# Kernel optimization log

Hardware: AMD Instinct MI355X
Metric: run time of the kernel (lower is better)

The kernel has to match this reference:

```python
import jax, jax.numpy as jnp
import numpy as np

N = 10000      # nodes
E = 160000     # edges (before self-loops)
H = 2          # ATTN_HEADS
D_IN = 256
C1 = 256       # hidden_channels per head in conv1
C2 = 512       # per-head channels in conv2 (hardcoded 512 in module)
OUT = 3


def setup_inputs():
    key = jax.random.key(0)
    ks = jax.random.split(key, 20)
    rn = lambda k, s, sc=0.05: jax.random.normal(k, s, jnp.float32) * sc
    return {
        "x": jax.random.normal(ks[0], (N, D_IN), jnp.float32),
        "edge_index": jax.random.randint(ks[1], (2, E), 0, N),
        # conv1: lin_src/lin_dst [D_IN, H*C1], attention vecs [H, C1], bias [H*C1]
        "w1s": rn(ks[2], (D_IN, H * C1)), "w1d": rn(ks[3], (D_IN, H * C1)),
        "a1s": rn(ks[4], (H, C1)), "a1d": rn(ks[5], (H, C1)), "b1": rn(ks[6], (H * C1,)),
        # conv2: input dim H*C1 -> [H*C1, H*C2]
        "w2s": rn(ks[7], (H * C1, H * C2)), "w2d": rn(ks[8], (H * C1, H * C2)),
        "a2s": rn(ks[9], (H, C2)), "a2d": rn(ks[10], (H, C2)), "b2": rn(ks[11], (H * C2,)),
        # MLP head
        "wf1": rn(ks[12], (H * C2, 128)), "bf1": rn(ks[13], (128,)),
        "gamma": jnp.ones((128,), jnp.float32), "beta": jnp.zeros((128,), jnp.float32),
        "wf2": rn(ks[14], (128, OUT)), "bf2": rn(ks[15], (OUT,)),
    }


def gat_layer(x, src, dst, Ws, Wd, att_s, att_d, b, n):
    h, c = att_s.shape
    xs = (x @ Ws).reshape(n, h, c)                      # [N,H,C] source messages
    xd = (x @ Wd).reshape(n, h, c)
    a_s = (xs * att_s).sum(-1)                          # [N,H]
    a_d = (xd * att_d).sum(-1)
    e = a_s[src] + a_d[dst]                             # [E,H]
    e = jnp.where(e > 0, e, 0.2 * e)                    # leaky_relu(0.2)
    m = jax.lax.stop_gradient(jax.ops.segment_max(e, dst, num_segments=n))
    alpha = jnp.exp(e - m[dst])
    denom = jax.ops.segment_sum(alpha, dst, num_segments=n)
    alpha = alpha / denom[dst]                          # segment softmax over dst
    out = jax.ops.segment_sum(xs[src] * alpha[..., None], dst, num_segments=n)
    return out.reshape(n, h * c) + b                    # concat heads + bias


def reference(x, edge_index, w1s, w1d, a1s, a1d, b1, w2s, w2d, a2s, a2d, b2,
              wf1, bf1, gamma, beta, wf2, bf2):
    loops = jnp.arange(N, dtype=edge_index.dtype)
    src = jnp.concatenate([edge_index[0], loops])       # add self-loops (PyG default)
    dst = jnp.concatenate([edge_index[1], loops])
    h = jax.nn.relu(gat_layer(x, src, dst, w1s, w1d, a1s, a1d, b1, N))
    h = jax.nn.relu(gat_layer(h, src, dst, w2s, w2d, a2s, a2d, b2, N))
    h = h @ wf1 + bf1
    mean = h.mean(0)
    var = ((h - mean) ** 2).mean(0)
    h = gamma * (h - mean) * jax.lax.rsqrt(var + 1e-5) + beta
    h = jax.nn.relu(h)
    h = h @ wf2 + bf2
    return jax.nn.log_softmax(h, axis=-1)
```

## Files before the change

kernel.cpp:

```cpp
#include <hip/hip_runtime.h>
#include <cstdint>
#include <cstddef>


typedef unsigned short u16;
typedef __bf16 bf16x8 __attribute__((ext_vector_type(8)));
typedef float f32x4 __attribute__((ext_vector_type(4)));
typedef unsigned short u16x8 __attribute__((ext_vector_type(8)));

__device__ __forceinline__ u16 f2b(float f) {
  union { float f; uint32_t u; } c; c.f = f;
  uint32_t u = c.u;
  return (u16)((u + 0x7FFFu + ((u >> 16) & 1u)) >> 16);
}
__device__ __forceinline__ float b2f(u16 h) {
  union { uint32_t u; float f; } c; c.u = ((uint32_t)h) << 16;
  return c.f;
}

__device__ __forceinline__ void async16(const void* g, void* l) {
  __builtin_amdgcn_global_load_lds((const __attribute__((address_space(1))) void*)g,
                                   (__attribute__((address_space(3))) void*)l, 16, 0, 0);
}

__device__ __forceinline__ float2 edge_w(const float4& as, const float4& ad) {
  float e0 = as.x + ad.z; e0 = e0 > 0.f ? e0 : 0.2f * e0;
  float e1 = as.y + ad.w; e1 = e1 > 0.f ? e1 : 0.2f * e1;
  return make_float2(__expf(e0), __expf(e1));
}

__device__ __forceinline__ void transpose_tile(const float* __restrict__ W, u16* __restrict__ WT,
                                               int K, int NC, int b, int t,
                                               u16 (*tile)[66]) {
  int tn = NC >> 6;
  int ti = b / tn, tj = b - ti * tn;
  int col = t & 63, r0 = t >> 6;
  const float* src = W + (size_t)(ti * 64) * NC + tj * 64;
#pragma unroll
  for (int i = 0; i < 16; i++) {
    int r = r0 + i * 4;
    tile[r][col] = f2b(src[(size_t)r * NC + col]);
  }
  __syncthreads();
  u16* dst = WT + (size_t)(tj * 64) * K + ti * 64;
#pragma unroll
  for (int i = 0; i < 16; i++) {
    int r = r0 + i * 4;
    dst[(size_t)r * K + col] = tile[col][r];
  }
}

__global__ __launch_bounds__(256) void prep(
    const float* __restrict__ x,
    const float* __restrict__ w1s, const float* __restrict__ w1d,
    const float* __restrict__ w2s, const float* __restrict__ w2d,
    const float* __restrict__ wf1,
    const float* __restrict__ a1s, const float* __restrict__ a1d,
    const float* __restrict__ a2s, const float* __restrict__ a2d,
    u16* __restrict__ xb, u16* __restrict__ w1T, u16* __restrict__ w2T,
    u16* __restrict__ wf1T, float* __restrict__ V1, float* __restrict__ V2,
    uint32_t* __restrict__ arena, int arena_nwords, int za,
    uint32_t* __restrict__ g1pad, int g1w, int zg1,
    uint32_t* __restrict__ g2pad, int g2w,
    int N) {
  __shared__ u16 tile[64][66];
  int b = blockIdx.x, t = threadIdx.x;
  const int R0 = 32;
  const int R1 = R0 + 128;
  const int R2 = R1 + 32;
  const int R3 = R2 + 256;
  const int R4 = R3 + 512;
  const int R5 = R4 + N / 4;
  const int R6 = R5 + za;
  const int R7 = R6 + zg1;

  if (b < R0) {
    transpose_tile(w1s, w1T, 256, 512, b, t, tile);
  } else if (b < R1) {
    transpose_tile(w2s, w2T, 512, 1024, b - R0, t, tile);
  } else if (b < R2) {
    transpose_tile(wf1, wf1T, 1024, 128, b - R1, t, tile);
  } else if (b < R3) {
    int wv = t >> 6, lane = t & 63;
    int u = (b - R2) * 4 + wv;
    int k = u >> 2, which = (u >> 1) & 1, h = u & 1;
    const float* W = which ? w1d : w1s;
    const float* att = which ? a1d : a1s;
    float s = 0.f;
#pragma unroll
    for (int c = lane; c < 256; c += 64) s += W[k * 512 + h * 256 + c] * att[h * 256 + c];
#pragma unroll
    for (int o = 32; o > 0; o >>= 1) s += __shfl_down(s, o);
    if (lane == 0) V1[k * 4 + which * 2 + h] = s;
  } else if (b < R4) {
    int wv = t >> 6, lane = t & 63;
    int u = (b - R3) * 4 + wv;
    int k = u >> 2, which = (u >> 1) & 1, h = u & 1;
    const float* W = which ? w2d : w2s;
    const float* att = which ? a2d : a2s;
    float s = 0.f;
#pragma unroll
    for (int c = lane; c < 512; c += 64) s += W[k * 1024 + h * 512 + c] * att[h * 512 + c];
#pragma unroll
    for (int o = 32; o > 0; o >>= 1) s += __shfl_down(s, o);
    if (lane == 0) V2[k * 4 + which * 2 + h] = s;
  } else if (b < R5) {
    int r = (b - R4) * 4 + (t >> 6);
    int c = (t & 63) * 4;
    float4 xv = *(const float4*)(x + (size_t)r * 256 + c);
    ushort4 st;
    st.x = f2b(xv.x); st.y = f2b(xv.y); st.z = f2b(xv.z); st.w = f2b(xv.w);
    *(ushort4*)(xb + (size_t)r * 256 + c) = st;
  } else if (b < R6) {
    int idx = (b - R5) * 256 + t;
    if (idx < arena_nwords) arena[idx] = 0u;
  } else if (b < R7) {
    int idx = (b - R6) * 256 + t;
    if (idx < g1w) g1pad[idx] = 0u;
  } else {
    int idx = (b - R7) * 256 + t;
    if (idx < g2w) g2pad[idx] = 0u;
  }
}

__global__ __launch_bounds__(256) void fill_a(const int* __restrict__ srcs,
                                              const int* __restrict__ dsts,
                                              int* __restrict__ cursor, int* __restrict__ csr,
                                              const float* __restrict__ X,
                                              const float* __restrict__ V,
                                              float* __restrict__ A, int N, int E, int FB) {
  int b = blockIdx.x, t = threadIdx.x;
  if (b < FB) {
    int i = b * 256 + t;
    if (i < N) {
      csr[(size_t)i * 64] = i;
    } else if (i < N + E) {
      int e = i - N;
      int d = dsts[e];
      int slot = atomicAdd(&cursor[d], 1) + 1;
      if (slot < 64) csr[(size_t)d * 64 + slot] = srcs[e];
    }
    return;
  }
  int node = (b - FB) * 4 + (t >> 6);
  int lane = t & 63;
  if (node >= N) return;
  const float* xr = X + (size_t)node * 256;
  float s0 = 0, s1 = 0, s2 = 0, s3 = 0;
  {
    int k = lane * 4;
    float4 xv = *(const float4*)(xr + k);
    float xe[4] = {xv.x, xv.y, xv.z, xv.w};
#pragma unroll
    for (int j = 0; j < 4; j++) {
      float4 v = ((const float4*)V)[k + j];
      s0 += xe[j] * v.x; s1 += xe[j] * v.y; s2 += xe[j] * v.z; s3 += xe[j] * v.w;
    }
  }
#pragma unroll
  for (int o = 32; o > 0; o >>= 1) {
    s0 += __shfl_down(s0, o); s1 += __shfl_down(s1, o);
    s2 += __shfl_down(s2, o); s3 += __shfl_down(s3, o);
  }
  if (lane == 0) ((float4*)A)[node] = make_float4(s0, s1, s2, s3);
}

__global__ __launch_bounds__(256) void agg1(const u16* __restrict__ xs,
                                            const float* __restrict__ a,
                                            const int* __restrict__ cursor,
                                            const int* __restrict__ csr,
                                            u16* __restrict__ g, int N) {
  int v = blockIdx.x * 8 + (threadIdx.x >> 5);
  if (v >= N) return;
  int c0 = (threadIdx.x & 31) * 8;
  const int* seg = csr + (size_t)v * 64;
  int cnt = min(cursor[v], 63) + 1;
  const float4* a4 = (const float4*)a;
  float4 adv = a4[v];
  float h0[8], h1[8];
#pragma unroll
  for (int j = 0; j < 8; j++) { h0[j] = 0.f; h1[j] = 0.f; }
  float den0 = 0.f, den1 = 0.f;

  auto body = [&](int4 s4) {
    float4 aa0 = a4[s4.x], aa1 = a4[s4.y], aa2 = a4[s4.z], aa3 = a4[s4.w];
    u16x8 x0 = *(const u16x8*)(xs + (size_t)s4.x * 256 + c0);
    u16x8 x1 = *(const u16x8*)(xs + (size_t)s4.y * 256 + c0);
    u16x8 x2 = *(const u16x8*)(xs + (size_t)s4.z * 256 + c0);
    u16x8 x3 = *(const u16x8*)(xs + (size_t)s4.w * 256 + c0);
    float2 w0 = edge_w(aa0, adv), w1 = edge_w(aa1, adv);
    float2 w2 = edge_w(aa2, adv), w3 = edge_w(aa3, adv);
    den0 += w0.x + w1.x + w2.x + w3.x;
    den1 += w0.y + w1.y + w2.y + w3.y;
#pragma unroll
    for (int j = 0; j < 8; j++) {
      float f0 = b2f(x0[j]), f1 = b2f(x1[j]), f2 = b2f(x2[j]), f3 = b2f(x3[j]);
      h0[j] += w0.x * f0 + w1.x * f1 + w2.x * f2 + w3.x * f3;
      h1[j] += w0.y * f0 + w1.y * f1 + w2.y * f2 + w3.y * f3;
    }
  };

  int nb4 = cnt & ~3;
  int i = 0;
  if (nb4 > 0) {
    int4 s4 = *(const int4*)(seg);
    for (i = 4; i < nb4; i += 4) {
      int4 nxt = *(const int4*)(seg + i);
      body(s4);
      s4 = nxt;
    }
    body(s4);
    i = nb4;
  }
  for (; i < cnt; i++) {
    int s = seg[i];
    float2 w = edge_w(a4[s], adv);
    den0 += w.x; den1 += w.y;
    u16x8 xv = *(const u16x8*)(xs + (size_t)s * 256 + c0);
#pragma unroll
    for (int j = 0; j < 8; j++) {
      float f = b2f(xv[j]);
      h0[j] += w.x * f;
      h1[j] += w.y * f;
    }
  }
  float r0 = 1.f / den0, r1 = 1.f / den1;
  u16x8 o0v, o1v;
#pragma unroll
  for (int j = 0; j < 8; j++) {
    o0v[j] = f2b(h0[j] * r0);
    o1v[j] = f2b(h1[j] * r1);
  }
  u16* grow = g + (size_t)v * 512;
  *(u16x8*)(grow + c0) = o0v;
  *(u16x8*)(grow + 256 + c0) = o1v;
}

__global__ __launch_bounds__(256) void agg2(const u16* __restrict__ xs,
                                            const float* __restrict__ a,
                                            const int* __restrict__ cursor,
                                            const int* __restrict__ csr,
                                            u16* __restrict__ g, int N) {
  int v = blockIdx.x * 4 + (threadIdx.x >> 6);
  if (v >= N) return;
  int c0 = (threadIdx.x & 63) * 8;
  const int* seg = csr + (size_t)v * 64;
  int cnt = min(cursor[v], 63) + 1;
  const float4* a4 = (const float4*)a;
  float4 adv = a4[v];
  float h0[8], h1[8];
#pragma unroll
  for (int j = 0; j < 8; j++) { h0[j] = 0.f; h1[j] = 0.f; }
  float den0 = 0.f, den1 = 0.f;

  auto body = [&](int4 s4) {
    float4 aa0 = a4[s4.x], aa1 = a4[s4.y], aa2 = a4[s4.z], aa3 = a4[s4.w];
    u16x8 x0 = *(const u16x8*)(xs + (size_t)s4.x * 512 + c0);
    u16x8 x1 = *(const u16x8*)(xs + (size_t)s4.y * 512 + c0);
    u16x8 x2 = *(const u16x8*)(xs + (size_t)s4.z * 512 + c0);
    u16x8 x3 = *(const u16x8*)(xs + (size_t)s4.w * 512 + c0);
    float2 w0 = edge_w(aa0, adv), w1 = edge_w(aa1, adv);
    float2 w2 = edge_w(aa2, adv), w3 = edge_w(aa3, adv);
    den0 += w0.x + w1.x + w2.x + w3.x;
    den1 += w0.y + w1.y + w2.y + w3.y;
#pragma unroll
    for (int j = 0; j < 8; j++) {
      float f0 = b2f(x0[j]), f1 = b2f(x1[j]), f2 = b2f(x2[j]), f3 = b2f(x3[j]);
      h0[j] += w0.x * f0 + w1.x * f1 + w2.x * f2 + w3.x * f3;
      h1[j] += w0.y * f0 + w1.y * f1 + w2.y * f2 + w3.y * f3;
    }
  };

  int nb4 = cnt & ~3;
  int i = 0;
  if (nb4 > 0) {
    int4 s4 = *(const int4*)(seg);
    for (i = 4; i < nb4; i += 4) {
      int4 nxt = *(const int4*)(seg + i);
      body(s4);
      s4 = nxt;
    }
    body(s4);
    i = nb4;
  }
  for (; i < cnt; i++) {
    int s = seg[i];
    float2 w = edge_w(a4[s], adv);
    den0 += w.x; den1 += w.y;
    u16x8 xv = *(const u16x8*)(xs + (size_t)s * 512 + c0);
#pragma unroll
    for (int j = 0; j < 8; j++) {
      float f = b2f(xv[j]);
      h0[j] += w.x * f;
      h1[j] += w.y * f;
    }
  }
  float r0 = 1.f / den0, r1 = 1.f / den1;
  u16x8 o0v, o1v;
#pragma unroll
  for (int j = 0; j < 8; j++) {
    o0v[j] = f2b(h0[j] * r0);
    o1v[j] = f2b(h1[j] * r1);
  }
  u16* grow = g + (size_t)v * 1024;
  *(u16x8*)(grow + c0) = o0v;
  *(u16x8*)(grow + 512 + c0) = o1v;
}

template <bool A2OUT>
__global__ __launch_bounds__(256) void gemm_bf16(const u16* __restrict__ A, int lda, int aZ,
                                                 const u16* __restrict__ BT, int ldb, int bZ,
                                                 const float* __restrict__ bias, int biasZ,
                                                 void* __restrict__ Cv, int ldc,
                                                 size_t cZ, int K, float* __restrict__ a2out,
                                                 const float* __restrict__ Vfold) {
  __shared__ u16 Asl[2][128 * 32];
  __shared__ u16 Bsl[2][128 * 32];
  int tid = threadIdx.x;
  int wave = tid >> 6, lane = tid & 63;
  int wr = wave >> 1, wc = wave & 1;
  int lr = lane & 15, quad = lane >> 4;
  size_t row0 = (size_t)blockIdx.y * 128;
  size_t n0 = (size_t)blockIdx.x * 128;
  int zq = blockIdx.z;
  A += (size_t)zq * aZ;
  BT += (size_t)zq * bZ;
  bias += (size_t)zq * biasZ;

  f32x4 acc[4][4];
#pragma unroll
  for (int i = 0; i < 4; i++)
#pragma unroll
    for (int j = 0; j < 4; j++) acc[i][j] = (f32x4){0.f, 0.f, 0.f, 0.f};

  int ra = tid >> 2;
  int ca = (tid & 3) * 8;
  const u16* gA = A + (row0 + ra) * lda + ca;
  const u16* gB = BT + (n0 + ra) * ldb + ca;
  int lbase = (tid & 192) * 8;

  async16(gA, &Asl[0][lbase]);
  async16(gA + (size_t)64 * lda, &Asl[0][lbase + 2048]);
  async16(gB, &Bsl[0][lbase]);
  async16(gB + (size_t)64 * ldb, &Bsl[0][lbase + 2048]);
  __syncthreads();

  int nIter = K >> 5;
  for (int it = 0; it < nIter; it++) {
    int cur = it & 1;
    if (it + 1 < nIter) {
      int kn = (it + 1) * 32;
      async16(gA + kn, &Asl[1 - cur][lbase]);
      async16(gA + (size_t)64 * lda + kn, &Asl[1 - cur][lbase + 2048]);
      async16(gB + kn, &Bsl[1 - cur][lbase]);
      async16(gB + (size_t)64 * ldb + kn, &Bsl[1 - cur][lbase + 2048]);
    }
    bf16x8 av[4], bv[4];
#pragma unroll
    for (int i = 0; i < 4; i++)
      av[i] = *(const bf16x8*)&Asl[cur][(wr * 64 + i * 16 + lr) * 32 + quad * 8];
#pragma unroll
    for (int j = 0; j < 4; j++)
      bv[j] = *(const bf16x8*)&Bsl[cur][(wc * 64 + j * 16 + lr) * 32 + quad * 8];
#pragma unroll
    for (int i = 0; i < 4; i++)
#pragma unroll
      for (int j = 0; j < 4; j++)
        acc[i][j] = __builtin_amdgcn_mfma_f32_16x16x32_bf16(av[i], bv[j], acc[i][j], 0, 0, 0);
    __syncthreads();
  }

  size_t crow = row0 + wr * 64 + quad * 4;
  size_t ccol = n0 + wc * 64 + lr;
  float bj[4];
#pragma unroll
  for (int j = 0; j < 4; j++) bj[j] = bias[ccol + j * 16];
  float4 vr[4];
  if (A2OUT) {
#pragma unroll
    for (int j = 0; j < 4; j++)
      vr[j] = ((const float4*)Vfold)[(size_t)zq * cZ + ccol + j * 16];
  }
  u16* C = (u16*)Cv + (size_t)zq * cZ;
#pragma unroll
  for (int i = 0; i < 4; i++) {
#pragma unroll
    for (int r = 0; r < 4; r++) {
      float pa0 = 0.f, pa1 = 0.f, pa2 = 0.f, pa3 = 0.f;
#pragma unroll
      for (int j = 0; j < 4; j++) {
        float val = fmaxf(acc[i][j][r] + bj[j], 0.f);
        C[(crow + i * 16 + r) * ldc + ccol + j * 16] = f2b(val);
        if (A2OUT) {
          pa0 += val * vr[j].x; pa1 += val * vr[j].y;
          pa2 += val * vr[j].z; pa3 += val * vr[j].w;
        }
      }
      if (A2OUT) {
#pragma unroll
        for (int o = 8; o > 0; o >>= 1) {
          pa0 += __shfl_down(pa0, o); pa1 += __shfl_down(pa1, o);
          pa2 += __shfl_down(pa2, o); pa3 += __shfl_down(pa3, o);
        }
        if (lr == 0) {
          float* ap = a2out + (crow + i * 16 + r) * 4;
          atomicAdd(ap + 0, pa0); atomicAdd(ap + 1, pa1);
          atomicAdd(ap + 2, pa2); atomicAdd(ap + 3, pa3);
        }
      }
    }
  }
}

__global__ __launch_bounds__(256) void gemm3_head(
    const u16* __restrict__ A, const u16* __restrict__ BT,
    float* __restrict__ sums, unsigned int* __restrict__ ctr,
    const float* __restrict__ gamma, const float* __restrict__ beta,
    const float* __restrict__ wf2, const float* __restrict__ bf2,
    float* __restrict__ out, int N, int nBlocks) {
  __shared__ u16 Asl[2][64 * 32];
  __shared__ u16 Bsl[2][128 * 32];
  __shared__ float part[2][64][3];
  int tid = threadIdx.x;
  int wave = tid >> 6, lane = tid & 63;
  int wr = wave >> 1, wc = wave & 1;
  int lr = lane & 15, quad = lane >> 4;
  size_t row0 = (size_t)blockIdx.x * 64;

  f32x4 acc[2][4];
#pragma unroll
  for (int i = 0; i < 2; i++)
#pragma unroll
    for (int j = 0; j < 4; j++) acc[i][j] = (f32x4){0.f, 0.f, 0.f, 0.f};

  const u16* gA = A + (row0 + (tid >> 2)) * 1024 + (tid & 3) * 8;
  const u16* gB = BT + (size_t)(tid >> 2) * 1024 + (tid & 3) * 8;
  int lb = (tid & 192) * 8;

  async16(gA, &Asl[0][lb]);
  async16(gB, &Bsl[0][lb]);
  async16(gB + 64 * 1024, &Bsl[0][2048 + lb]);
  __syncthreads();

  for (int it = 0; it < 32; it++) {
    int cur = it & 1;
    if (it + 1 < 32) {
      int kn = (it + 1) * 32;
      async16(gA + kn, &Asl[1 - cur][lb]);
      async16(gB + kn, &Bsl[1 - cur][lb]);
      async16(gB + 64 * 1024 + kn, &Bsl[1 - cur][2048 + lb]);
    }
    bf16x8 av[2], bv[4];
#pragma unroll
    for (int i = 0; i < 2; i++)
      av[i] = *(const bf16x8*)&Asl[cur][(wr * 32 + i * 16 + lr) * 32 + quad * 8];
#pragma unroll
    for (int j = 0; j < 4; j++)
      bv[j] = *(const bf16x8*)&Bsl[cur][(wc * 64 + j * 16 + lr) * 32 + quad * 8];
#pragma unroll
    for (int i = 0; i < 2; i++)
#pragma unroll
      for (int j = 0; j < 4; j++)
        acc[i][j] = __builtin_amdgcn_mfma_f32_16x16x32_bf16(av[i], bv[j], acc[i][j], 0, 0, 0);
    __syncthreads();
  }

  int ccol = wc * 64 + lr;
  float s1[4] = {0.f, 0.f, 0.f, 0.f}, s2[4] = {0.f, 0.f, 0.f, 0.f};
#pragma unroll
  for (int i = 0; i < 2; i++)
#pragma unroll
    for (int r = 0; r < 4; r++) {
      int row = (int)row0 + wr * 32 + i * 16 + quad * 4 + r;
      if (row < N) {
#pragma unroll
        for (int j = 0; j < 4; j++) {
          float v = acc[i][j][r];
          s1[j] += v; s2[j] += v * v;
        }
      }
    }
#pragma unroll
  for (int j = 0; j < 4; j++) {
#pragma unroll
    for (int o = 16; o < 64; o <<= 1) {
      s1[j] += __shfl_down(s1[j], o);
      s2[j] += __shfl_down(s2[j], o);
    }
  }
  if (quad == 0) {
#pragma unroll
    for (int j = 0; j < 4; j++) {
      atomicAdd(&sums[ccol + j * 16], s1[j]);
      atomicAdd(&sums[128 + ccol + j * 16], s2[j]);
    }
  }

  __syncthreads();
  if (tid == 0) {
    __threadfence();
    atomicAdd(ctr, 1u);
    while (__hip_atomic_load(ctr, __ATOMIC_ACQUIRE, __HIP_MEMORY_SCOPE_AGENT) <
           (unsigned)nBlocks) {
    }
  }
  __syncthreads();

  float inv = 1.f / (float)N;
  float mean[4], rstd[4], gm[4], bt[4], w3[4][3];
#pragma unroll
  for (int j = 0; j < 4; j++) {
    int col = ccol + j * 16;
    float sv = __hip_atomic_load(&sums[col], __ATOMIC_RELAXED, __HIP_MEMORY_SCOPE_AGENT);
    float qv = __hip_atomic_load(&sums[128 + col], __ATOMIC_RELAXED, __HIP_MEMORY_SCOPE_AGENT);
    mean[j] = sv * inv;
    float var = qv * inv - mean[j] * mean[j];
    rstd[j] = rsqrtf(var + 1e-5f);
    gm[j] = gamma[col]; bt[j] = beta[col];
    w3[j][0] = wf2[col * 3 + 0]; w3[j][1] = wf2[col * 3 + 1]; w3[j][2] = wf2[col * 3 + 2];
  }
#pragma unroll
  for (int i = 0; i < 2; i++)
#pragma unroll
    for (int r = 0; r < 4; r++) {
      float p0 = 0.f, p1 = 0.f, p2 = 0.f;
#pragma unroll
      for (int j = 0; j < 4; j++) {
        float h = gm[j] * (acc[i][j][r] - mean[j]) * rstd[j] + bt[j];
        h = fmaxf(h, 0.f);
        p0 += h * w3[j][0]; p1 += h * w3[j][1]; p2 += h * w3[j][2];
      }
#pragma unroll
      for (int o = 8; o > 0; o >>= 1) {
        p0 += __shfl_down(p0, o); p1 += __shfl_down(p1, o); p2 += __shfl_down(p2, o);
      }
      if (lr == 0) {
        int lrow = wr * 32 + i * 16 + quad * 4 + r;
        part[wc][lrow][0] = p0; part[wc][lrow][1] = p1; part[wc][lrow][2] = p2;
      }
    }
  __syncthreads();
  if (tid < 64) {
    int row = tid;
    if ((int)row0 + row < N) {
      float l0 = part[0][row][0] + part[1][row][0] + bf2[0];
      float l1 = part[0][row][1] + part[1][row][1] + bf2[1];
      float l2 = part[0][row][2] + part[1][row][2] + bf2[2];
      float mx = fmaxf(l0, fmaxf(l1, l2));
      float lse = mx + logf(__expf(l0 - mx) + __expf(l1 - mx) + __expf(l2 - mx));
      float* orow = out + ((size_t)row0 + row) * 3;
      orow[0] = l0 - lse; orow[1] = l1 - lse; orow[2] = l2 - lse;
    }
  }
}

extern "C" void kernel_launch(void* const* d_in, const int* in_sizes, int n_in,
                              void* d_out, int out_size, void* d_ws, size_t ws_size,
                              hipStream_t stream) {
  const float* x     = (const float*)d_in[0];
  const int*   ei    = (const int*)d_in[1];
  const float* w1s   = (const float*)d_in[2];
  const float* w1d   = (const float*)d_in[3];
  const float* a1s   = (const float*)d_in[4];
  const float* a1d   = (const float*)d_in[5];
  const float* b1    = (const float*)d_in[6];
  const float* w2s   = (const float*)d_in[7];
  const float* w2d   = (const float*)d_in[8];
  const float* a2s   = (const float*)d_in[9];
  const float* a2d   = (const float*)d_in[10];
  const float* b2    = (const float*)d_in[11];
  const float* wf1   = (const float*)d_in[12];
  const float* gamma = (const float*)d_in[14];
  const float* beta  = (const float*)d_in[15];
  const float* wf2   = (const float*)d_in[16];
  const float* bf2   = (const float*)d_in[17];
  float* out = (float*)d_out;

  const int N = in_sizes[0] / 256;
  const int E = in_sizes[1] / 2;
  const int Mpad = ((N + 127) / 128) * 128;
  (void)n_in; (void)out_size; (void)ws_size;

  char* ws = (char*)d_ws;
  size_t off = 0;
  auto alloc = [&](size_t bytes) -> char* {
    off = (off + 255) & ~(size_t)255;
    char* p = ws + off;
    off += bytes;
    return p;
  };
  u16* xb    = (u16*)alloc((size_t)N * 256 * 2);
  u16* w1T   = (u16*)alloc((size_t)512 * 256 * 2);
  u16* w2T   = (u16*)alloc((size_t)1024 * 512 * 2);
  u16* wf1T  = (u16*)alloc((size_t)128 * 1024 * 2);
  u16* g1    = (u16*)alloc((size_t)Mpad * 512 * 2);
  u16* h1    = (u16*)alloc((size_t)Mpad * 512 * 2);
  u16* g2    = (u16*)alloc((size_t)Mpad * 1024 * 2);
  u16* h2    = (u16*)alloc((size_t)Mpad * 1024 * 2);
  float* a1  = (float*)alloc((size_t)N * 16);
  float* V1  = (float*)alloc(256 * 16);
  float* V2  = (float*)alloc(512 * 16);
  int* csr   = (int*)alloc((size_t)N * 64 * 4);
  size_t curB = (size_t)N * 4;
  size_t a2B = (size_t)Mpad * 16;
  size_t arenaB = curB + a2B + 1024 + 256;
  char* arena = alloc(arenaB);
  int* cursor = (int*)arena;
  float* a2   = (float*)(arena + curB);
  float* sums = (float*)(arena + curB + a2B);
  unsigned int* ctr = (unsigned int*)(sums + 256);

  int arena_nwords = (int)(arenaB / 4);
  int za  = (arena_nwords + 255) / 256;
  int g1w = (Mpad - N) * 512 * 2 / 4;
  int zg1 = (g1w + 255) / 256;
  int g2w = (Mpad - N) * 1024 * 2 / 4;
  int zg2 = (g2w + 255) / 256;
  int prep_blocks = 32 + 128 + 32 + 256 + 512 + N / 4 + za + zg1 + zg2;

  prep<<<prep_blocks, 256, 0, stream>>>(
      x, w1s, w1d, w2s, w2d, wf1, a1s, a1d, a2s, a2d,
      xb, w1T, w2T, wf1T, V1, V2,
      (uint32_t*)arena, arena_nwords, za,
      (uint32_t*)(g1 + (size_t)N * 512), g1w, zg1,
      (uint32_t*)(g2 + (size_t)N * 1024), g2w, N);

  const int* srcs = ei;
  const int* dsts = ei + E;

  int FB = (N + E + 255) / 256;
  fill_a<<<FB + (N + 3) / 4, 256, 0, stream>>>(srcs, dsts, cursor, csr, x, V1, a1, N, E, FB);

  int mt = Mpad / 128;

  agg1<<<(N + 7) / 8, 256, 0, stream>>>(xb, a1, cursor, csr, g1, N);
  gemm_bf16<true><<<dim3(2, mt, 2), 256, 0, stream>>>(
      g1, 512, 256, w1T, 256, 256 * 256, b1, 256, h1, 512, 256, 256, a2, V2);
  agg2<<<(N + 3) / 4, 256, 0, stream>>>(h1, a2, cursor, csr, g2, N);
  gemm_bf16<false><<<dim3(4, mt, 2), 256, 0, stream>>>(
      g2, 1024, 512, w2T, 512, 512 * 512, b2, 512, h2, 1024, 512, 512, nullptr, nullptr);
  int nB3 = Mpad / 64;
  gemm3_head<<<nB3, 256, 0, stream>>>(h2, wf1T, sums, ctr, gamma, beta, wf2, bf2, out, N, nB3);
}
```

Baseline: 233.1 us.

## Fuse conv2 GEMM and MLP head into one producer-consumer kernel launch

Merges the second GAT GEMM and the head GEMM/batchnorm/log-softmax kernel into a single launch. Producer blocks compute h2 tiles and bump a global done counter, while consumer blocks prefetch their wf1 tiles, then spin until every producer has finished before reading h2. The aim is to remove one kernel launch gap and let consumers stage weights early. The cost is that consumers spin while holding compute units, which relies on all producers being scheduled ahead of them to avoid deadlock. The unused template parameter on gemm_bf16 is also dropped.

```diff
diff --git a/kernel.cpp b/kernel.cpp
--- a/kernel.cpp
+++ b/kernel.cpp
@@ -307,7 +307,6 @@
   *(u16x8*)(grow + 512 + c0) = o1v;
 }
 
-template <bool A2OUT>
 __global__ __launch_bounds__(256) void gemm_bf16(const u16* __restrict__ A, int lda, int aZ,
                                                  const u16* __restrict__ BT, int ldb, int bZ,
                                                  const float* __restrict__ bias, int biasZ,
@@ -376,11 +375,9 @@
 #pragma unroll
   for (int j = 0; j < 4; j++) bj[j] = bias[ccol + j * 16];
   float4 vr[4];
-  if (A2OUT) {
-#pragma unroll
-    for (int j = 0; j < 4; j++)
-      vr[j] = ((const float4*)Vfold)[(size_t)zq * cZ + ccol + j * 16];
-  }
+#pragma unroll
+  for (int j = 0; j < 4; j++)
+    vr[j] = ((const float4*)Vfold)[(size_t)zq * cZ + ccol + j * 16];
   u16* C = (u16*)Cv + (size_t)zq * cZ;
 #pragma unroll
   for (int i = 0; i < 4; i++) {
@@ -391,41 +388,120 @@
       for (int j = 0; j < 4; j++) {
         float val = fmaxf(acc[i][j][r] + bj[j], 0.f);
         C[(crow + i * 16 + r) * ldc + ccol + j * 16] = f2b(val);
-        if (A2OUT) {
-          pa0 += val * vr[j].x; pa1 += val * vr[j].y;
-          pa2 += val * vr[j].z; pa3 += val * vr[j].w;
-        }
+        pa0 += val * vr[j].x; pa1 += val * vr[j].y;
+        pa2 += val * vr[j].z; pa3 += val * vr[j].w;
       }
-      if (A2OUT) {
-#pragma unroll
-        for (int o = 8; o > 0; o >>= 1) {
-          pa0 += __shfl_down(pa0, o); pa1 += __shfl_down(pa1, o);
-          pa2 += __shfl_down(pa2, o); pa3 += __shfl_down(pa3, o);
-        }
-        if (lr == 0) {
-          float* ap = a2out + (crow + i * 16 + r) * 4;
-          atomicAdd(ap + 0, pa0); atomicAdd(ap + 1, pa1);
-          atomicAdd(ap + 2, pa2); atomicAdd(ap + 3, pa3);
-        }
+#pragma unroll
+      for (int o = 8; o > 0; o >>= 1) {
+        pa0 += __shfl_down(pa0, o); pa1 += __shfl_down(pa1, o);
+        pa2 += __shfl_down(pa2, o); pa3 += __shfl_down(pa3, o);
       }
-    }
-  }
-}
-
-__global__ __launch_bounds__(256) void gemm3_head(
-    const u16* __restrict__ A, const u16* __restrict__ BT,
-    float* __restrict__ sums, unsigned int* __restrict__ ctr,
+      if (lr == 0) {
+        float* ap = a2out + (crow + i * 16 + r) * 4;
+        atomicAdd(ap + 0, pa0); atomicAdd(ap + 1, pa1);
+        atomicAdd(ap + 2, pa2); atomicAdd(ap + 3, pa3);
+      }
+    }
+  }
+}
+
+__global__ __launch_bounds__(256, 4) void gemm23(
+    const u16* __restrict__ g2, const u16* __restrict__ w2T,
+    const float* __restrict__ b2, u16* __restrict__ h2,
+    const u16* __restrict__ wf1T, float* __restrict__ sums,
+    unsigned int* __restrict__ ctr, unsigned int* __restrict__ done,
     const float* __restrict__ gamma, const float* __restrict__ beta,
     const float* __restrict__ wf2, const float* __restrict__ bf2,
-    float* __restrict__ out, int N, int nBlocks) {
-  __shared__ u16 Asl[2][64 * 32];
-  __shared__ u16 Bsl[2][128 * 32];
-  __shared__ float part[2][64][3];
+    float* __restrict__ out, int N, int mt, int nProd, int nCons) {
+  __shared__ __align__(16) char smem[32768];
+  int b = blockIdx.x;
   int tid = threadIdx.x;
   int wave = tid >> 6, lane = tid & 63;
   int wr = wave >> 1, wc = wave & 1;
   int lr = lane & 15, quad = lane >> 4;
-  size_t row0 = (size_t)blockIdx.x * 64;
+  int lb = (tid & 192) * 8;
+
+  if (b < nProd) {
+    u16* Asl = (u16*)smem;
+    u16* Bsl = (u16*)(smem + 16384);
+    int xq = b & 3;
+    int t2 = b >> 2;
+    int yq = t2 % mt;
+    int zq = t2 / mt;
+    size_t row0 = (size_t)yq * 128;
+    size_t n0 = (size_t)xq * 128;
+    const u16* A = g2 + (size_t)zq * 512;
+    const u16* BT = w2T + (size_t)zq * (512 * 512);
+    const float* bias = b2 + zq * 512;
+
+    f32x4 acc[4][4];
+#pragma unroll
+    for (int i = 0; i < 4; i++)
+#pragma unroll
+      for (int j = 0; j < 4; j++) acc[i][j] = (f32x4){0.f, 0.f, 0.f, 0.f};
+
+    int ra = tid >> 2;
+    int ca = (tid & 3) * 8;
+    const u16* gA = A + (row0 + ra) * 1024 + ca;
+    const u16* gB = BT + (n0 + ra) * 512 + ca;
+
+    async16(gA, &Asl[lb]);
+    async16(gA + (size_t)64 * 1024, &Asl[lb + 2048]);
+    async16(gB, &Bsl[lb]);
+    async16(gB + (size_t)64 * 512, &Bsl[lb + 2048]);
+    __syncthreads();
+
+    for (int it = 0; it < 16; it++) {
+      int cur = it & 1;
+      if (it + 1 < 16) {
+        int kn = (it + 1) * 32;
+        async16(gA + kn, &Asl[(1 - cur) * 4096 + lb]);
+        async16(gA + (size_t)64 * 1024 + kn, &Asl[(1 - cur) * 4096 + lb + 2048]);
+        async16(gB + kn, &Bsl[(1 - cur) * 4096 + lb]);
+        async16(gB + (size_t)64 * 512 + kn, &Bsl[(1 - cur) * 4096 + lb + 2048]);
+      }
+      bf16x8 av[4], bv[4];
+#pragma unroll
+      for (int i = 0; i < 4; i++)
+        av[i] = *(const bf16x8*)&Asl[cur * 4096 + (wr * 64 + i * 16 + lr) * 32 + quad * 8];
+#pragma unroll
+      for (int j = 0; j < 4; j++)
+        bv[j] = *(const bf16x8*)&Bsl[cur * 4096 + (wc * 64 + j * 16 + lr) * 32 + quad * 8];
+#pragma unroll
+      for (int i = 0; i < 4; i++)
+#pragma unroll
+        for (int j = 0; j < 4; j++)
+          acc[i][j] = __builtin_amdgcn_mfma_f32_16x16x32_bf16(av[i], bv[j], acc[i][j], 0, 0, 0);
+      __syncthreads();
+    }
+
+    size_t crow = row0 + wr * 64 + quad * 4;
+    size_t ccol = n0 + wc * 64 + lr;
+    float bj[4];
+#pragma unroll
+    for (int j = 0; j < 4; j++) bj[j] = bias[ccol + j * 16];
+    u16* C = h2 + (size_t)zq * 512;
+#pragma unroll
+    for (int i = 0; i < 4; i++)
+#pragma unroll
+      for (int r = 0; r < 4; r++)
+#pragma unroll
+        for (int j = 0; j < 4; j++)
+          C[(crow + i * 16 + r) * 1024 + ccol + j * 16] =
+              f2b(fmaxf(acc[i][j][r] + bj[j], 0.f));
+    __syncthreads();
+    if (tid == 0) {
+      __threadfence();
+      __hip_atomic_fetch_add(done, 1u, __ATOMIC_RELEASE, __HIP_MEMORY_SCOPE_AGENT);
+    }
+    return;
+  }
+
+  u16* Asl = (u16*)smem;
+  u16* Bsl = (u16*)(smem + 8192);
+  float* part = (float*)(smem + 24576);
+  int b3 = b - nProd;
+  size_t row0 = (size_t)b3 * 64;
 
   f32x4 acc[2][4];
 #pragma unroll
@@ -433,30 +509,36 @@
 #pragma unroll
     for (int j = 0; j < 4; j++) acc[i][j] = (f32x4){0.f, 0.f, 0.f, 0.f};
 
-  const u16* gA = A + (row0 + (tid >> 2)) * 1024 + (tid & 3) * 8;
-  const u16* gB = BT + (size_t)(tid >> 2) * 1024 + (tid & 3) * 8;
-  int lb = (tid & 192) * 8;
-
-  async16(gA, &Asl[0][lb]);
-  async16(gB, &Bsl[0][lb]);
-  async16(gB + 64 * 1024, &Bsl[0][2048 + lb]);
+  const u16* gA = h2 + (row0 + (tid >> 2)) * 1024 + (tid & 3) * 8;
+  const u16* gB = wf1T + (size_t)(tid >> 2) * 1024 + (tid & 3) * 8;
+
+  async16(gB, &Bsl[lb]);
+  async16(gB + 64 * 1024, &Bsl[2048 + lb]);
+  if (tid == 0) {
+    while (__hip_atomic_load(done, __ATOMIC_ACQUIRE, __HIP_MEMORY_SCOPE_AGENT) <
+           (unsigned)nProd) {
+      __builtin_amdgcn_s_sleep(8);
+    }
+  }
+  __syncthreads();
+  async16(gA, &Asl[lb]);
   __syncthreads();
 
   for (int it = 0; it < 32; it++) {
     int cur = it & 1;
     if (it + 1 < 32) {
       int kn = (it + 1) * 32;
-      async16(gA + kn, &Asl[1 - cur][lb]);
-      async16(gB + kn, &Bsl[1 - cur][lb]);
-      async16(gB + 64 * 1024 + kn, &Bsl[1 - cur][2048 + lb]);
+      async16(gA + kn, &Asl[(1 - cur) * 2048 + lb]);
+      async16(gB + kn, &Bsl[(1 - cur) * 4096 + lb]);
+      async16(gB + 64 * 1024 + kn, &Bsl[(1 - cur) * 4096 + 2048 + lb]);
     }
     bf16x8 av[2], bv[4];
 #pragma unroll
     for (int i = 0; i < 2; i++)
-      av[i] = *(const bf16x8*)&Asl[cur][(wr * 32 + i * 16 + lr) * 32 + quad * 8];
+      av[i] = *(const bf16x8*)&Asl[cur * 2048 + (wr * 32 + i * 16 + lr) * 32 + quad * 8];
 #pragma unroll
     for (int j = 0; j < 4; j++)
-      bv[j] = *(const bf16x8*)&Bsl[cur][(wc * 64 + j * 16 + lr) * 32 + quad * 8];
+      bv[j] = *(const bf16x8*)&Bsl[cur * 4096 + (wc * 64 + j * 16 + lr) * 32 + quad * 8];
 #pragma unroll
     for (int i = 0; i < 2; i++)
 #pragma unroll
@@ -501,7 +583,7 @@
     __threadfence();
     atomicAdd(ctr, 1u);
     while (__hip_atomic_load(ctr, __ATOMIC_ACQUIRE, __HIP_MEMORY_SCOPE_AGENT) <
-           (unsigned)nBlocks) {
+           (unsigned)nCons) {
     }
   }
   __syncthreads();
@@ -536,16 +618,18 @@
       }
       if (lr == 0) {
         int lrow = wr * 32 + i * 16 + quad * 4 + r;
-        part[wc][lrow][0] = p0; part[wc][lrow][1] = p1; part[wc][lrow][2] = p2;
+        part[(wc * 64 + lrow) * 3 + 0] = p0;
+        part[(wc * 64 + lrow) * 3 + 1] = p1;
+        part[(wc * 64 + lrow) * 3 + 2] = p2;
       }
     }
   __syncthreads();
   if (tid < 64) {
     int row = tid;
     if ((int)row0 + row < N) {
-      float l0 = part[0][row][0] + part[1][row][0] + bf2[0];
-      float l1 = part[0][row][1] + part[1][row][1] + bf2[1];
-      float l2 = part[0][row][2] + part[1][row][2] + bf2[2];
+      float l0 = part[row * 3 + 0] + part[(64 + row) * 3 + 0] + bf2[0];
+      float l1 = part[row * 3 + 1] + part[(64 + row) * 3 + 1] + bf2[1];
+      float l2 = part[row * 3 + 2] + part[(64 + row) * 3 + 2] + bf2[2];
       float mx = fmaxf(l0, fmaxf(l1, l2));
       float lse = mx + logf(__expf(l0 - mx) + __expf(l1 - mx) + __expf(l2 - mx));
       float* orow = out + ((size_t)row0 + row) * 3;
@@ -608,7 +692,8 @@
   int* cursor = (int*)arena;
   float* a2   = (float*)(arena + curB);
   float* sums = (float*)(arena + curB + a2B);
-  unsigned int* ctr = (unsigned int*)(sums + 256);
+  unsigned int* ctr  = (unsigned int*)(sums + 256);
+  unsigned int* done = ctr + 1;
 
   int arena_nwords = (int)(arenaB / 4);
   int za  = (arena_nwords + 255) / 256;
@@ -634,11 +719,11 @@
   int mt = Mpad / 128;
 
   agg1<<<(N + 7) / 8, 256, 0, stream>>>(xb, a1, cursor, csr, g1, N);
-  gemm_bf16<true><<<dim3(2, mt, 2), 256, 0, stream>>>(
+  gemm_bf16<<<dim3(2, mt, 2), 256, 0, stream>>>(
       g1, 512, 256, w1T, 256, 256 * 256, b1, 256, h1, 512, 256, 256, a2, V2);
   agg2<<<(N + 3) / 4, 256, 0, stream>>>(h1, a2, cursor, csr, g2, N);
-  gemm_bf16<false><<<dim3(4, mt, 2), 256, 0, stream>>>(
-      g2, 1024, 512, w2T, 512, 512 * 512, b2, 512, h2, 1024, 512, 512, nullptr, nullptr);
-  int nB3 = Mpad / 64;
-  gemm3_head<<<nB3, 256, 0, stream>>>(h2, wf1T, sums, ctr, gamma, beta, wf2, bf2, out, N, nB3);
-}
+  int nProd = 4 * mt * 2;
+  int nCons = Mpad / 64;
+  gemm23<<<nProd + nCons, 256, 0, stream>>>(
+      g2, w2T, b2, h2, wf1T, sums, ctr, done, gamma, beta, wf2, bf2, out, N, mt, nProd, nCons);
+}
```

Result: slower. 349.5 us (+49.9%).
